# Performance work log

Measured on AMD Instinct MI355X. Metric: run time of the kernel, lower is better.

The kernel has to match this reference:

```python
import jax, jax.numpy as jnp
import numpy as np

NB, NLOC, NALL, NNEI, A_SEL = 1, 512, 640, 96, 20
N_DIM, E_DIM, A_DIM, AXIS = 128, 64, 64, 4
EDGE_INFO = 2 * N_DIM + E_DIM          # 320
SYM = AXIS * (E_DIM + N_DIM)           # 768, cal_1_dim
ANGLE = A_DIM + N_DIM + 2 * E_DIM      # 320, angle_dim


def setup_inputs() -> dict:
    key = jax.random.key(0)
    ks = jax.random.split(key, 16)
    nrm = lambda k, sh, s=1.0: jax.random.normal(k, sh, dtype=jnp.float32) * s

    def lin(k, din, dout, s=0.05):
        k1, k2 = jax.random.split(k)
        return nrm(k1, (din, dout), s), nrm(k2, (dout,), s)

    inp = {}
    inp["g1_ext"] = nrm(ks[0], (NB, NALL, N_DIM))
    inp["g2"] = nrm(ks[1], (NB, NLOC, NNEI, E_DIM))
    inp["h2"] = nrm(ks[2], (NB, NLOC, NNEI, 3))
    inp["angle_embed"] = nrm(ks[3], (NB, NLOC, A_SEL, A_SEL, A_DIM))
    inp["sw"] = jax.random.uniform(ks[4], (NB, NLOC, NNEI), dtype=jnp.float32)
    inp["a_sw"] = jax.random.uniform(ks[5], (NB, NLOC, A_SEL), dtype=jnp.float32)
    inp["w_self"], inp["b_self"] = lin(ks[6], N_DIM, N_DIM)
    inp["w_proj"] = nrm(ks[7], (E_DIM, N_DIM), 0.05)  # proj_g1g2, bias=False
    inp["w_lin1"], inp["b_lin1"] = lin(ks[8], SYM, N_DIM)
    inp["w_edge1"], inp["b_edge1"] = lin(ks[9], EDGE_INFO, N_DIM)
    inp["w_lin2"], inp["b_lin2"] = lin(ks[10], EDGE_INFO, E_DIM)
    inp["w_ang"], inp["b_ang"] = lin(ks[11], ANGLE, A_DIM)
    inp["w_ga1"], inp["b_ga1"] = lin(ks[12], ANGLE, E_DIM)
    inp["w_ga2"], inp["b_ga2"] = lin(ks[13], E_DIM, E_DIM)
    inp["nlist"] = jax.random.randint(ks[14], (NB, NLOC, NNEI), 0, NALL)
    inp["nlist_mask"] = jnp.ones((NB, NLOC, NNEI), dtype=bool)
    inp["a_nlist_mask"] = jnp.ones((NB, NLOC, A_SEL), dtype=bool)
    return inp


def _sym_op(g, h2, mask, sw, axis):
    # symmetrization_op: _cal_hg (smooth, use_sqrt_nnei) followed by _cal_grrg
    # g: nb x nloc x nnei x d, h2: nb x nloc x nnei x 3
    g = jnp.where(mask[..., None], g, 0.0) * sw[..., None]
    inv = np.float32(1.0 / np.sqrt(g.shape[2]))
    hg = jnp.einsum('blnt,blnd->bltd', h2, g) * inv
    grrg = jnp.einsum('bltd,blta->blda', hg, hg[..., :axis])  # nb x nloc x d x axis
    return grrg.reshape(grrg.shape[0], grrg.shape[1], -1)


def reference(g1_ext, g2, h2, angle_embed, sw, a_sw,
              w_self, b_self, w_proj, w_lin1, b_lin1, w_edge1, b_edge1,
              w_lin2, b_lin2, w_ang, b_ang, w_ga1, b_ga1, w_ga2, b_ga2,
              nlist, nlist_mask, a_nlist_mask):
    act = jax.nn.silu
    nb, nloc, nnei, e_dim = g2.shape
    n_dim = g1_ext.shape[-1]
    a_sel = angle_embed.shape[2]
    g1 = g1_ext[:, :nloc]
    # _make_nei_g1: gather neighbor node features, nb x nloc x nnei x n_dim
    gg1 = jnp.take_along_axis(
        g1_ext, nlist.reshape(nb, nloc * nnei, 1), axis=1
    ).reshape(nb, nloc, nnei, n_dim)
    maskf = nlist_mask[..., None]
    swf = sw[..., None]

    g1_update = [g1]
    # node self mlp
    g1_update.append(act(g1 @ w_self + b_self))
    # conv update: masked+switched gg1 times projected g2, mean over nnei
    gg1_ms = jnp.where(maskf, gg1, 0.0) * swf
    g1_update.append(jnp.sum((g2 @ w_proj) * gg1_ms, axis=2) / np.float32(nnei))
    # symmetrized axis-neuron update
    sym = jnp.concatenate(
        [_sym_op(g2, h2, nlist_mask, sw, AXIS),
         _sym_op(gg1, h2, nlist_mask, sw, AXIS)], axis=-1)
    g1_update.append(act(sym @ w_lin1 + b_lin1))
    # edge info: [tiled g1, gg1, g2] -> 2*n_dim + e_dim
    edge_info = jnp.concatenate(
        [jnp.broadcast_to(g1[:, :, None, :], (nb, nloc, nnei, n_dim)), gg1, g2],
        axis=-1)
    g1_edge = act(edge_info @ w_edge1 + b_edge1) * swf
    g1_update.append(jnp.sum(g1_edge, axis=2) / np.float32(nnei))
    # res_avg
    g1_new = sum(g1_update) / np.float32(np.sqrt(len(g1_update)))

    g2_update = [g2, act(edge_info @ w_lin2 + b_lin2)]

    # angle branch: angle_dim = a_dim + n_dim + 2*e_dim
    g2a = jnp.where(a_nlist_mask[..., None], g2[:, :, :a_sel, :], 0.0)
    ang = jnp.concatenate([
        angle_embed,
        jnp.broadcast_to(g1[:, :, None, None, :], (nb, nloc, a_sel, a_sel, n_dim)),
        jnp.broadcast_to(g2a[:, :, :, None, :], (nb, nloc, a_sel, a_sel, e_dim)),
        jnp.broadcast_to(g2a[:, :, None, :, :], (nb, nloc, a_sel, a_sel, e_dim)),
    ], axis=-1)
    a_new = (angle_embed + act(ang @ w_ang + b_ang)) / np.float32(np.sqrt(2.0))

    # angle -> edge message, switch-weighted on both angle axes, mean over one axis
    ang_w = ang * a_sw[:, :, :, None, None] * a_sw[:, :, None, :, None]
    g2_ang = jnp.sum(act(ang_w @ w_ga1 + b_ga1), axis=3) / np.float32(a_sel)
    g2_ang_full = jnp.concatenate(
        [g2_ang, jnp.zeros((nb, nloc, nnei - a_sel, e_dim), g2.dtype)], axis=2)
    g2_update.append(act(g2_ang_full @ w_ga2 + b_ga2))
    g2_new = sum(g2_update) / np.float32(np.sqrt(len(g2_update)))

    return g1_new, g2_new, h2, a_new
```

## Files before the change

kernel.cpp:

```cpp
#include <hip/hip_runtime.h>
#include <hip/hip_bf16.h>

#define NLOC 512
#define NALL 640
#define NNEI 96
#define ASEL 20
#define NDIM 128
#define EDIM 64
#define ADIM 64

typedef short bf16x8 __attribute__((ext_vector_type(8)));
typedef float f32x4 __attribute__((ext_vector_type(4)));
typedef unsigned short ushort8 __attribute__((ext_vector_type(8)));
typedef unsigned short ushort4_t __attribute__((ext_vector_type(4)));

__device__ __forceinline__ unsigned short f2bf(float f) {
    unsigned int u = __float_as_uint(f);
    unsigned int r = (u + 0x7FFFu + ((u >> 16) & 1u)) >> 16;
    return (unsigned short)r;
}
__device__ __forceinline__ float bf2f(unsigned short u) {
    return __uint_as_float(((unsigned int)u) << 16);
}
__device__ __forceinline__ float silu(float x) { return x / (1.0f + __expf(-x)); }

__device__ __forceinline__ void cvt8_store(unsigned short* dst, const float* src) {
    float4 f0 = *(const float4*)src;
    float4 f1 = *(const float4*)(src + 4);
    ushort8 v;
    v[0] = f2bf(f0.x); v[1] = f2bf(f0.y); v[2] = f2bf(f0.z); v[3] = f2bf(f0.w);
    v[4] = f2bf(f1.x); v[5] = f2bf(f1.y); v[6] = f2bf(f1.z); v[7] = f2bf(f1.w);
    *(ushort8*)dst = v;
}

__device__ __forceinline__ f32x4 red16(f32x4 v) {
#pragma unroll
    for (int m = 1; m < 16; m <<= 1) {
        v[0] += __shfl_xor(v[0], m);
        v[1] += __shfl_xor(v[1], m);
        v[2] += __shfl_xor(v[2], m);
        v[3] += __shfl_xor(v[3], m);
    }
    return v;
}

__global__ void prep_bt2(const float* __restrict__ w_ang, const float* __restrict__ w_ga1,
                         const float* __restrict__ w_edge1, const float* __restrict__ w_lin2,
                         const float* __restrict__ w_proj, const float* __restrict__ w_self,
                         unsigned short* __restrict__ bt_ae, unsigned short* __restrict__ bt_g2e,
                         unsigned short* __restrict__ bt_sm, unsigned short* __restrict__ bt_pij) {
    int idx = blockIdx.x * 256 + threadIdx.x;
    if (idx < 8192) {
        int k = idx & 63, n = idx >> 6;
        bt_ae[idx] = f2bf((n < 64) ? w_ang[k * 64 + n] : w_ga1[k * 64 + (n - 64)]);
    } else if (idx < 32768) {
        int id2 = idx - 8192;
        int k = id2 & 63, n = id2 >> 6;
        float v;
        if (n < 128)      v = w_edge1[(256 + k) * 128 + n];
        else if (n < 192) v = w_lin2[(256 + k) * 64 + (n - 128)];
        else if (n < 256) v = 0.0f;
        else              v = w_proj[k * 128 + (n - 256)];
        bt_g2e[id2] = f2bf(v);
    } else if (idx < 114688) {
        int id3 = idx - 32768;
        int k = id3 & 127, n = id3 >> 7;
        float v;
        if (n < 128)      v = w_edge1[k * 128 + n];
        else if (n < 192) v = w_lin2[k * 64 + (n - 128)];
        else if (n < 320) v = w_edge1[(128 + k) * 128 + (n - 192)];
        else if (n < 384) v = w_lin2[(128 + k) * 64 + (n - 320)];
        else if (n < 512) { int c = n - 384;
            v = (c < 64) ? w_ang[(64 + k) * 64 + c] : w_ga1[(64 + k) * 64 + (c - 64)]; }
        else              v = w_self[k * 128 + (n - 512)];
        bt_sm[id3] = f2bf(v);
    } else {
        int id4 = idx - 114688;
        int k = id4 & 63, n = id4 >> 6;
        float v;
        if (n < 128) v = (n < 64) ? w_ang[(192 + k) * 64 + n] : w_ga1[(192 + k) * 64 + (n - 64)];
        else { int c = n - 128;
            v = (c < 64) ? w_ang[(256 + k) * 64 + c] : w_ga1[(256 + k) * 64 + (c - 64)]; }
        bt_pij[id4] = f2bf(v);
    }
}

__global__ __launch_bounds__(256) void gemm_small(
    const float* __restrict__ g1_ext, const unsigned short* __restrict__ bt_sm,
    const float* __restrict__ b_self, float* __restrict__ P1a, float* __restrict__ g1self,
    float* __restrict__ E1, float* __restrict__ E2) {
    const int m0 = blockIdx.x * 128;
    const int ntile = blockIdx.y;
    __shared__ __align__(16) unsigned short Asl[128 * 136];
    __shared__ __align__(16) unsigned short Bsl[128 * 136];
    const int tid = threadIdx.x;
#pragma unroll
    for (int u = 0; u < 8; u++) {
        int g = tid + u * 256;
        int row = g >> 4, seg = g & 15;
        cvt8_store(&Asl[row * 136 + seg * 8], g1_ext + (m0 + row) * 128 + seg * 8);
        *(ushort8*)&Bsl[row * 136 + seg * 8] =
            *(const ushort8*)&bt_sm[(ntile * 128 + row) * 128 + seg * 8];
    }
    __syncthreads();
    const int lane = tid & 63, wid = tid >> 6;
    const int wr = wid >> 1, wc = wid & 1;
    const int r15 = lane & 15, kg = lane >> 4;
    f32x4 acc[4][4] = {};
#pragma unroll
    for (int h = 0; h < 4; h++) {
        bf16x8 afr[4], bfr[4];
#pragma unroll
        for (int mi = 0; mi < 4; mi++)
            afr[mi] = *(const bf16x8*)&Asl[(wr * 64 + mi * 16 + r15) * 136 + h * 32 + kg * 8];
#pragma unroll
        for (int ni = 0; ni < 4; ni++)
            bfr[ni] = *(const bf16x8*)&Bsl[(wc * 64 + ni * 16 + r15) * 136 + h * 32 + kg * 8];
#pragma unroll
        for (int mi = 0; mi < 4; mi++)
#pragma unroll
            for (int ni = 0; ni < 4; ni++)
                acc[mi][ni] = __builtin_amdgcn_mfma_f32_16x16x32_bf16(afr[mi], bfr[ni], acc[mi][ni], 0, 0, 0);
    }
#pragma unroll
    for (int mi = 0; mi < 4; mi++) {
        int rbase = m0 + wr * 64 + mi * 16 + kg * 4;
#pragma unroll
        for (int ni = 0; ni < 4; ni++) {
            int gc = ntile * 128 + wc * 64 + ni * 16 + r15;
#pragma unroll
            for (int t2 = 0; t2 < 4; t2++) {
                int a = rbase + t2;
                float z = acc[mi][ni][t2];
                if (gc < 192) { if (a < 512) E1[a * 192 + gc] = z; }
                else if (gc < 384) E2[a * 192 + (gc - 192)] = z;
                else if (gc < 512) { if (a < 512) P1a[a * 128 + (gc - 384)] = z; }
                else { if (a < 512) g1self[a * 128 + (gc - 512)] = silu(z + b_self[gc - 512]); }
            }
        }
    }
}

__global__ __launch_bounds__(256) void gemm_pij(
    const float* __restrict__ g2, const unsigned short* __restrict__ bt_pij,
    unsigned short* __restrict__ P_i, unsigned short* __restrict__ P_j,
    unsigned short* __restrict__ P_jT) {
    const int m0 = blockIdx.x * 128;
    const int ntile = blockIdx.y;
    __shared__ __align__(16) unsigned short Asl[128 * 72];
    const int tid = threadIdx.x;
#pragma unroll
    for (int u = 0; u < 4; u++) {
        int g = tid + u * 256;
        int row = g >> 3, seg = g & 7;
        int li = m0 + row, l = li / 20, i = li - l * 20;
        cvt8_store(&Asl[row * 72 + seg * 8], g2 + (l * 96 + i) * 64 + seg * 8);
    }
    __syncthreads();
    const int lane = tid & 63, wid = tid >> 6;
    const int wr = wid >> 1, wc = wid & 1;
    const int r15 = lane & 15, kg = lane >> 4;
    f32x4 acc[4][4] = {};
#pragma unroll
    for (int h = 0; h < 2; h++) {
        bf16x8 afr[4], bfr[4];
#pragma unroll
        for (int mi = 0; mi < 4; mi++)
            afr[mi] = *(const bf16x8*)&Asl[(wr * 64 + mi * 16 + r15) * 72 + h * 32 + kg * 8];
#pragma unroll
        for (int ni = 0; ni < 4; ni++)
            bfr[ni] = *(const bf16x8*)&bt_pij[(ntile * 128 + wc * 64 + ni * 16 + r15) * 64 + h * 32 + kg * 8];
#pragma unroll
        for (int mi = 0; mi < 4; mi++)
#pragma unroll
            for (int ni = 0; ni < 4; ni++)
                acc[mi][ni] = __builtin_amdgcn_mfma_f32_16x16x32_bf16(afr[mi], bfr[ni], acc[mi][ni], 0, 0, 0);
    }
    unsigned short* Pout = (ntile == 0) ? P_i : P_j;
#pragma unroll
    for (int mi = 0; mi < 4; mi++) {
        int rbase = m0 + wr * 64 + mi * 16 + kg * 4;
#pragma unroll
        for (int ni = 0; ni < 4; ni++) {
            int c = wc * 64 + ni * 16 + r15;
#pragma unroll
            for (int t2 = 0; t2 < 4; t2++) {
                unsigned short v = f2bf(acc[mi][ni][t2]);
                int li = rbase + t2;
                Pout[li * 128 + c] = v;
                if (ntile == 1) {
                    int l = li / 20, j = li - l * 20;
                    P_jT[(l * 128 + c) * 20 + j] = v;
                }
            }
        }
    }
}

__global__ void k_sym(const float* __restrict__ g1_ext, const float* __restrict__ g2,
                      const float* __restrict__ h2, const float* __restrict__ sw,
                      const int* __restrict__ nlist, const float* __restrict__ w_lin1,
                      const float* __restrict__ b_lin1, float* __restrict__ term4) {
    int l = blockIdx.x, t = threadIdx.x;
    __shared__ float h2s[96 * 3];
    __shared__ float sws[96];
    __shared__ int nls[96];
    __shared__ float hg[3 * 192];
    __shared__ float symv[768];
    __shared__ float red[128];
    if (t < 96) { sws[t] = sw[l * 96 + t]; nls[t] = nlist[l * 96 + t]; }
    for (int p = t; p < 288; p += 256) h2s[p] = h2[l * 288 + p];
    __syncthreads();
    const float inv = 0.1020620726f;
    for (int p = t; p < 576; p += 256) {
        float acc = 0.0f;
        if (p < 192) {
            int tt = p >> 6, d = p & 63;
            for (int n = 0; n < 96; n++)
                acc += h2s[n * 3 + tt] * g2[(l * 96 + n) * 64 + d] * sws[n];
            hg[tt * 192 + d] = acc * inv;
        } else {
            int q = p - 192;
            int tt = q >> 7, d = q & 127;
            for (int n = 0; n < 96; n++)
                acc += h2s[n * 3 + tt] * g1_ext[nls[n] * 128 + d] * sws[n];
            hg[tt * 192 + 64 + d] = acc * inv;
        }
    }
    __syncthreads();
    for (int p = t; p < 768; p += 256) {
        float acc = 0.0f;
        if (p < 256) {
            int d = p >> 2, a = p & 3;
            for (int tt = 0; tt < 3; tt++) acc += hg[tt * 192 + d] * hg[tt * 192 + a];
        } else {
            int q = p - 256;
            int d = q >> 2, a = q & 3;
            for (int tt = 0; tt < 3; tt++) acc += hg[tt * 192 + 64 + d] * hg[tt * 192 + 64 + a];
        }
        symv[p] = acc;
    }
    __syncthreads();
    {
        int col = t & 127, half = t >> 7;
        float acc = 0.0f;
        int k0 = half * 384;
#pragma unroll 8
        for (int k = k0; k < k0 + 384; k++) acc += symv[k] * w_lin1[k * 128 + col];
        if (half) red[col] = acc;
        __syncthreads();
        if (!half) term4[l * 128 + col] = silu(acc + red[col] + b_lin1[col]);
    }
}

__global__ __launch_bounds__(256) void angle_main(
    const float* __restrict__ ae, const unsigned short* __restrict__ bt_ae,
    const float* __restrict__ P1a, const unsigned short* __restrict__ P_i,
    const unsigned short* __restrict__ P_j, const unsigned short* __restrict__ P_jT,
    const float* __restrict__ a_sw,
    const float* __restrict__ b_ang, const float* __restrict__ b_ga1,
    float* __restrict__ g2acc, float* __restrict__ a_new_out) {
    const int m0 = blockIdx.x * 64;
    __shared__ __align__(16) unsigned short Asl[64 * 72];
    const int tid = threadIdx.x;
#pragma unroll
    for (int u = 0; u < 2; u++) {
        int g = tid + u * 256;
        int row = g >> 3, seg = g & 7;
        cvt8_store(&Asl[row * 72 + seg * 8], ae + (m0 + row) * 64 + seg * 8);
    }
    __syncthreads();
    const int lane = tid & 63, wid = tid >> 6;
    const int r15 = lane & 15, kg = lane >> 4;
    f32x4 accA[4] = {};
    f32x4 accB[4] = {};
#pragma unroll
    for (int h = 0; h < 2; h++) {
        bf16x8 afr, bfrA[4], bfrB[4];
        afr = *(const bf16x8*)&Asl[(wid * 16 + r15) * 72 + h * 32 + kg * 8];
#pragma unroll
        for (int ni = 0; ni < 4; ni++) {
            bfrA[ni] = *(const bf16x8*)&bt_ae[(ni * 16 + r15) * 64 + h * 32 + kg * 8];
            bfrB[ni] = *(const bf16x8*)&bt_ae[(64 + ni * 16 + r15) * 64 + h * 32 + kg * 8];
        }
#pragma unroll
        for (int ni = 0; ni < 4; ni++) {
            accA[ni] = __builtin_amdgcn_mfma_f32_16x16x32_bf16(bfrA[ni], afr, accA[ni], 0, 0, 0);
            accB[ni] = __builtin_amdgcn_mfma_f32_16x16x32_bf16(afr, bfrB[ni], accB[ni], 0, 0, 0);
        }
    }
    {
        int r = m0 + wid * 16 + r15;
        int l = r / 400;
        int rem = r - l * 400;
        int i = rem / 20;
        int j = rem - i * 20;
        const float* p1b = P1a + l * 128;
        const unsigned short* pib = P_i + (l * 20 + i) * 128;
        const unsigned short* pjb = P_j + (l * 20 + j) * 128;
        int lr = r - m0;
#pragma unroll
        for (int ni = 0; ni < 4; ni++) {
            int n0 = ni * 16 + kg * 4;
            f32x4 p1v = *(const f32x4*)&p1b[n0];
            ushort4_t piv = *(const ushort4_t*)&pib[n0];
            ushort4_t pjv = *(const ushort4_t*)&pjb[n0];
            ushort4_t aev = *(const ushort4_t*)&Asl[lr * 72 + n0];
            f32x4 bbv = *(const f32x4*)&b_ang[n0];
            f32x4 outv;
#pragma unroll
            for (int t2 = 0; t2 < 4; t2++) {
                float z = accA[ni][t2] + p1v[t2] + bf2f(piv[t2]) + bf2f(pjv[t2]);
                outv[t2] = (bf2f(aev[t2]) + silu(z + bbv[t2])) * 0.70710678f;
            }
            *(f32x4*)&a_new_out[r * 64 + n0] = outv;
        }
    }
    {
        int rbase = m0 + wid * 16 + kg * 4;
        int l = rbase / 400;
        int rem = rbase - l * 400;
        int i = rem / 20;
        int j0 = rem - i * 20;
        const float* p1b = P1a + l * 128;
        const unsigned short* pib = P_i + (l * 20 + i) * 128;
        float swi = a_sw[l * 20 + i];
        f32x4 swjv = *(const f32x4*)&a_sw[l * 20 + j0];
#pragma unroll
        for (int ni = 0; ni < 4; ni++) {
            int c = 64 + ni * 16 + r15;
            int cc = c - 64;
            float base = p1b[c] + bf2f(pib[c]);
            float bb = b_ga1[cc];
            ushort4_t pjtv = *(const ushort4_t*)&P_jT[(l * 128 + c) * 20 + j0];
            float part = 0.0f;
#pragma unroll
            for (int t2 = 0; t2 < 4; t2++) {
                float z = accB[ni][t2] + base + bf2f(pjtv[t2]);
                part += silu(swi * swjv[t2] * z + bb);
            }
            atomicAdd(&g2acc[(l * 20 + i) * 64 + cc], part);
        }
    }
}

__global__ void k_f2(const float* __restrict__ g2ang_acc, const float* __restrict__ w_ga2,
                     const float* __restrict__ b_ga2, float* __restrict__ yga2) {
    int l = blockIdx.x, t = threadIdx.x;
    __shared__ float gs[20 * 64];
    for (int p = t; p < 1280; p += 256) gs[p] = g2ang_acc[l * 1280 + p] * 0.05f;
    __syncthreads();
    for (int p = t; p < 1280; p += 256) {
        int i = p >> 6, c = p & 63;
        float acc = b_ga2[c];
#pragma unroll 8
        for (int k = 0; k < 64; k++) acc += gs[i * 64 + k] * w_ga2[k * 64 + c];
        yga2[l * 1280 + p] = silu(acc);
    }
}

__global__ __launch_bounds__(256) void edge_main(
    const float* __restrict__ g1_ext, const float* __restrict__ g2, const float* __restrict__ sw,
    const int* __restrict__ nlist, const unsigned short* __restrict__ bt_g2e,
    const float* __restrict__ E1, const float* __restrict__ E2,
    const float* __restrict__ b_edge1, const float* __restrict__ b_lin2,
    const float* __restrict__ b_ga2, const float* __restrict__ yga2,
    float* __restrict__ g1_acc3, float* __restrict__ g1_acc5, float* __restrict__ g2_new_out) {
    const int m0 = blockIdx.x * 128;
    const int ntile = blockIdx.y;
    __shared__ __align__(16) unsigned short Asl[128 * 72];
    const int tid = threadIdx.x;
#pragma unroll
    for (int u = 0; u < 4; u++) {
        int g = tid + u * 256;
        int row = g >> 3, seg = g & 7;
        cvt8_store(&Asl[row * 72 + seg * 8], g2 + (m0 + row) * 64 + seg * 8);
    }
    __syncthreads();
    const int lane = tid & 63, wid = tid >> 6;
    const int r15 = lane & 15, kg = lane >> 4;
    if (ntile == 1) {
        f32x4 acc[2][4] = {};
#pragma unroll
        for (int h = 0; h < 2; h++) {
            bf16x8 afr[2], bfr[4];
#pragma unroll
            for (int mi = 0; mi < 2; mi++)
                afr[mi] = *(const bf16x8*)&Asl[(wid * 32 + mi * 16 + r15) * 72 + h * 32 + kg * 8];
#pragma unroll
            for (int ni = 0; ni < 4; ni++)
                bfr[ni] = *(const bf16x8*)&bt_g2e[(128 + ni * 16 + r15) * 64 + h * 32 + kg * 8];
#pragma unroll
            for (int mi = 0; mi < 2; mi++)
#pragma unroll
                for (int ni = 0; ni < 4; ni++)
                    acc[mi][ni] = __builtin_amdgcn_mfma_f32_16x16x32_bf16(bfr[ni], afr[mi], acc[mi][ni], 0, 0, 0);
        }
#pragma unroll
        for (int mi = 0; mi < 2; mi++) {
            int r = m0 + wid * 32 + mi * 16 + r15;
            int l = r / 96;
            int nn = r - l * 96;
            const float* e1 = E1 + l * 192 + 128;
            const float* e2 = E2 + nlist[r] * 192 + 128;
            bool hasyg = (nn < ASEL);
            const float* yg = yga2 + (l * 20 + nn) * 64;
            int lr = r - m0;
#pragma unroll
            for (int ni = 0; ni < 4; ni++) {
                int n0 = ni * 16 + kg * 4;
                f32x4 e1v = *(const f32x4*)&e1[n0];
                f32x4 e2v = *(const f32x4*)&e2[n0];
                f32x4 bbv = *(const f32x4*)&b_lin2[n0];
                f32x4 bg2 = *(const f32x4*)&b_ga2[n0];
                ushort4_t g2v = *(const ushort4_t*)&Asl[lr * 72 + n0];
                f32x4 outv;
#pragma unroll
                for (int t2 = 0; t2 < 4; t2++) {
                    float z = acc[mi][ni][t2] + e1v[t2] + e2v[t2];
                    float y = silu(z + bbv[t2]);
                    float ygv = hasyg ? yg[n0 + t2] : silu(bg2[t2]);
                    outv[t2] = (bf2f(g2v[t2]) + y + ygv) * 0.57735027f;
                }
                *(f32x4*)&g2_new_out[r * 64 + n0] = outv;
            }
        }
    } else {
        const int bn = (ntile == 0) ? 0 : 256;
        f32x4 acc[2][8] = {};
#pragma unroll
        for (int h = 0; h < 2; h++) {
            bf16x8 afr[2], bfr[8];
#pragma unroll
            for (int mi = 0; mi < 2; mi++)
                afr[mi] = *(const bf16x8*)&Asl[(wid * 32 + mi * 16 + r15) * 72 + h * 32 + kg * 8];
#pragma unroll
            for (int ni = 0; ni < 8; ni++)
                bfr[ni] = *(const bf16x8*)&bt_g2e[(bn + ni * 16 + r15) * 64 + h * 32 + kg * 8];
#pragma unroll
            for (int mi = 0; mi < 2; mi++)
#pragma unroll
                for (int ni = 0; ni < 8; ni++)
                    acc[mi][ni] = __builtin_amdgcn_mfma_f32_16x16x32_bf16(bfr[ni], afr[mi], acc[mi][ni], 0, 0, 0);
        }
#pragma unroll
        for (int mi = 0; mi < 2; mi++) {
            int r = m0 + wid * 32 + mi * 16 + r15;
            int l = r / 96;
            float swr = sw[r];
            int nr = nlist[r];
            if (ntile == 0) {
                const float* e1 = E1 + l * 192;
                const float* e2 = E2 + nr * 192;
#pragma unroll
                for (int ni = 0; ni < 8; ni++) {
                    int n0 = ni * 16 + kg * 4;
                    f32x4 e1v = *(const f32x4*)&e1[n0];
                    f32x4 e2v = *(const f32x4*)&e2[n0];
                    f32x4 bbv = *(const f32x4*)&b_edge1[n0];
                    f32x4 p;
#pragma unroll
                    for (int t2 = 0; t2 < 4; t2++)
                        p[t2] = silu(acc[mi][ni][t2] + e1v[t2] + e2v[t2] + bbv[t2]) * swr;
                    p = red16(p);
                    if (r15 == 0) {
#pragma unroll
                        for (int t2 = 0; t2 < 4; t2++)
                            atomicAdd(&g1_acc5[l * 128 + n0 + t2], p[t2]);
                    }
                }
            } else {
                const float* gv = g1_ext + nr * 128;
#pragma unroll
                for (int ni = 0; ni < 8; ni++) {
                    int n0 = ni * 16 + kg * 4;
                    f32x4 g4 = *(const f32x4*)&gv[n0];
                    f32x4 p;
#pragma unroll
                    for (int t2 = 0; t2 < 4; t2++)
                        p[t2] = acc[mi][ni][t2] * g4[t2] * swr;
                    p = red16(p);
                    if (r15 == 0) {
#pragma unroll
                        for (int t2 = 0; t2 < 4; t2++)
                            atomicAdd(&g1_acc3[l * 128 + n0 + t2], p[t2]);
                    }
                }
            }
        }
    }
}

__global__ void k_f1(const float* __restrict__ g1_ext, const float* __restrict__ g1self,
                     const float* __restrict__ acc3, const float* __restrict__ term4,
                     const float* __restrict__ acc5, const float* __restrict__ h2,
                     float* __restrict__ out_g1, float* __restrict__ out_h2) {
    int idx = blockIdx.x * 256 + threadIdx.x;
    float v = g1_ext[idx] + g1self[idx] + acc3[idx] * (1.0f / 96.0f) + term4[idx] +
              acc5[idx] * (1.0f / 96.0f);
    out_g1[idx] = v * 0.4472135955f;
    if (idx < 36864)
        *(float4*)&out_h2[idx * 4] = *(const float4*)&h2[idx * 4];
}

extern "C" void kernel_launch(void* const* d_in, const int* in_sizes, int n_in,
                              void* d_out, int out_size, void* d_ws, size_t ws_size,
                              hipStream_t stream) {
    if (n_in < 22 || in_sizes[0] != 81920 || in_sizes[3] != 13107200) return;
    const float* g1_ext = (const float*)d_in[0];
    const float* g2     = (const float*)d_in[1];
    const float* h2     = (const float*)d_in[2];
    const float* ae     = (const float*)d_in[3];
    const float* sw     = (const float*)d_in[4];
    const float* a_sw   = (const float*)d_in[5];
    const float* w_self = (const float*)d_in[6];
    const float* b_self = (const float*)d_in[7];
    const float* w_proj = (const float*)d_in[8];
    const float* w_lin1 = (const float*)d_in[9];
    const float* b_lin1 = (const float*)d_in[10];
    const float* w_edge1= (const float*)d_in[11];
    const float* b_edge1= (const float*)d_in[12];
    const float* w_lin2 = (const float*)d_in[13];
    const float* b_lin2 = (const float*)d_in[14];
    const float* w_ang  = (const float*)d_in[15];
    const float* b_ang  = (const float*)d_in[16];
    const float* w_ga1  = (const float*)d_in[17];
    const float* b_ga1  = (const float*)d_in[18];
    const float* w_ga2  = (const float*)d_in[19];
    const float* b_ga2  = (const float*)d_in[20];
    const int*   nlist  = (const int*)d_in[21];

    float* ws = (float*)d_ws;
    unsigned short* bt_ae  = (unsigned short*)(ws);
    unsigned short* bt_g2e = (unsigned short*)(ws + 4096);
    unsigned short* bt_sm  = (unsigned short*)(ws + 16384);
    unsigned short* bt_pij = (unsigned short*)(ws + 57344);
    float* P1a    = ws + 65536;
    float* E1     = ws + 131072;
    float* E2     = ws + 229376;
    unsigned short* P_i = (unsigned short*)(ws + 352256);
    unsigned short* P_j = (unsigned short*)(ws + 1007616);
    float* g1self = ws + 1662976;
    float* term4  = ws + 1728512;
    float* yga2   = ws + 1794048;
    float* acc3   = ws + 2449408;
    float* acc5   = ws + 2514944;
    float* g2acc  = ws + 2580480;
    unsigned short* P_jT = (unsigned short*)(ws + 3235840);
    if (ws_size < (size_t)3563520 * sizeof(float)) return;

    float* out = (float*)d_out;
    float* out_g1 = out;
    float* out_g2 = out + 65536;
    float* out_h2 = out + 3211264;
    float* out_an = out + 3358720;

    hipMemsetAsync(acc3, 0, (65536 + 65536 + 655360) * sizeof(float), stream);

    prep_bt2<<<512, 256, 0, stream>>>(w_ang, w_ga1, w_edge1, w_lin2, w_proj, w_self,
                                      bt_ae, bt_g2e, bt_sm, bt_pij);
    gemm_small<<<dim3(5, 5), 256, 0, stream>>>(g1_ext, bt_sm, b_self, P1a, g1self, E1, E2);
    gemm_pij<<<dim3(80, 2), 256, 0, stream>>>(g2, bt_pij, P_i, P_j, P_jT);
    k_sym<<<512, 256, 0, stream>>>(g1_ext, g2, h2, sw, nlist, w_lin1, b_lin1, term4);
    angle_main<<<3200, 256, 0, stream>>>(ae, bt_ae, P1a, P_i, P_j, P_jT, a_sw, b_ang, b_ga1,
                                         g2acc, out_an);
    k_f2<<<512, 256, 0, stream>>>(g2acc, w_ga2, b_ga2, yga2);
    edge_main<<<dim3(384, 3), 256, 0, stream>>>(g1_ext, g2, sw, nlist, bt_g2e, E1, E2,
                                                b_edge1, b_lin2, b_ga2, yga2,
                                                acc3, acc5, out_g2);
    k_f1<<<256, 256, 0, stream>>>(g1_ext, g1self, acc3, term4, acc5, h2, out_g1, out_h2);
}
```

Measured before the change: 166.9 us.

## Restructure angle kernel rows so each wave owns full i-rows, drop atomics

```diff
diff --git a/kernel.cpp b/kernel.cpp
--- a/kernel.cpp
+++ b/kernel.cpp
@@ -253,95 +253,105 @@
     }
 }
 
-__global__ __launch_bounds__(256) void angle_main(
+__global__ __launch_bounds__(128) void angle_main(
     const float* __restrict__ ae, const unsigned short* __restrict__ bt_ae,
     const float* __restrict__ P1a, const unsigned short* __restrict__ P_i,
     const unsigned short* __restrict__ P_j, const unsigned short* __restrict__ P_jT,
     const float* __restrict__ a_sw,
     const float* __restrict__ b_ang, const float* __restrict__ b_ga1,
     float* __restrict__ g2acc, float* __restrict__ a_new_out) {
-    const int m0 = blockIdx.x * 64;
-    __shared__ __align__(16) unsigned short Asl[64 * 72];
+    const int m0 = blockIdx.x * 160;
+    __shared__ __align__(16) unsigned short Asl[160 * 72];
     const int tid = threadIdx.x;
 #pragma unroll
-    for (int u = 0; u < 2; u++) {
-        int g = tid + u * 256;
-        int row = g >> 3, seg = g & 7;
-        cvt8_store(&Asl[row * 72 + seg * 8], ae + (m0 + row) * 64 + seg * 8);
-    }
-    __syncthreads();
-    const int lane = tid & 63, wid = tid >> 6;
+    for (int u = 0; u < 10; u++) {
+        int g = tid + u * 128;
+        int slot = g >> 3, seg = g & 7;
+        int chunk = slot / 80, s = slot - chunk * 80;
+        int t = s >> 4, w16 = s & 15;
+        int kg2 = w16 >> 2, t2s = w16 & 3;
+        int grow = m0 + chunk * 80 + kg2 * 20 + t * 4 + t2s;
+        cvt8_store(&Asl[slot * 72 + seg * 8], ae + grow * 64 + seg * 8);
+    }
+    __syncthreads();
+    const int lane = tid & 63, w = tid >> 6;
     const int r15 = lane & 15, kg = lane >> 4;
-    f32x4 accA[4] = {};
-    f32x4 accB[4] = {};
-#pragma unroll
-    for (int h = 0; h < 2; h++) {
-        bf16x8 afr, bfrA[4], bfrB[4];
-        afr = *(const bf16x8*)&Asl[(wid * 16 + r15) * 72 + h * 32 + kg * 8];
-#pragma unroll
-        for (int ni = 0; ni < 4; ni++) {
-            bfrA[ni] = *(const bf16x8*)&bt_ae[(ni * 16 + r15) * 64 + h * 32 + kg * 8];
-            bfrB[ni] = *(const bf16x8*)&bt_ae[(64 + ni * 16 + r15) * 64 + h * 32 + kg * 8];
-        }
-#pragma unroll
-        for (int ni = 0; ni < 4; ni++) {
-            accA[ni] = __builtin_amdgcn_mfma_f32_16x16x32_bf16(bfrA[ni], afr, accA[ni], 0, 0, 0);
-            accB[ni] = __builtin_amdgcn_mfma_f32_16x16x32_bf16(afr, bfrB[ni], accB[ni], 0, 0, 0);
-        }
-    }
-    {
-        int r = m0 + wid * 16 + r15;
-        int l = r / 400;
-        int rem = r - l * 400;
-        int i = rem / 20;
-        int j = rem - i * 20;
-        const float* p1b = P1a + l * 128;
-        const unsigned short* pib = P_i + (l * 20 + i) * 128;
-        const unsigned short* pjb = P_j + (l * 20 + j) * 128;
-        int lr = r - m0;
-#pragma unroll
-        for (int ni = 0; ni < 4; ni++) {
-            int n0 = ni * 16 + kg * 4;
-            f32x4 p1v = *(const f32x4*)&p1b[n0];
-            ushort4_t piv = *(const ushort4_t*)&pib[n0];
-            ushort4_t pjv = *(const ushort4_t*)&pjb[n0];
-            ushort4_t aev = *(const ushort4_t*)&Asl[lr * 72 + n0];
-            f32x4 bbv = *(const f32x4*)&b_ang[n0];
-            f32x4 outv;
-#pragma unroll
-            for (int t2 = 0; t2 < 4; t2++) {
-                float z = accA[ni][t2] + p1v[t2] + bf2f(piv[t2]) + bf2f(pjv[t2]);
-                outv[t2] = (bf2f(aev[t2]) + silu(z + bbv[t2])) * 0.70710678f;
-            }
-            *(f32x4*)&a_new_out[r * 64 + n0] = outv;
-        }
-    }
-    {
-        int rbase = m0 + wid * 16 + kg * 4;
-        int l = rbase / 400;
-        int rem = rbase - l * 400;
-        int i = rem / 20;
-        int j0 = rem - i * 20;
-        const float* p1b = P1a + l * 128;
-        const unsigned short* pib = P_i + (l * 20 + i) * 128;
-        float swi = a_sw[l * 20 + i];
-        f32x4 swjv = *(const f32x4*)&a_sw[l * 20 + j0];
-#pragma unroll
-        for (int ni = 0; ni < 4; ni++) {
-            int c = 64 + ni * 16 + r15;
-            int cc = c - 64;
-            float base = p1b[c] + bf2f(pib[c]);
-            float bb = b_ga1[cc];
-            ushort4_t pjtv = *(const ushort4_t*)&P_jT[(l * 128 + c) * 20 + j0];
-            float part = 0.0f;
-#pragma unroll
-            for (int t2 = 0; t2 < 4; t2++) {
-                float z = accB[ni][t2] + base + bf2f(pjtv[t2]);
-                part += silu(swi * swjv[t2] * z + bb);
-            }
-            atomicAdd(&g2acc[(l * 20 + i) * 64 + cc], part);
-        }
-    }
+    const int cb = m0 + w * 80;
+    const int l = cb / 400;
+    const int i0 = (cb - l * 400) / 20;
+    const int kgA = r15 >> 2, t2A = r15 & 3;
+    const int iA = i0 + kgA;
+    f32x4 p1vA[4], bbvA[4];
+    ushort4_t pivA[4];
+#pragma unroll
+    for (int ni = 0; ni < 4; ni++) {
+        int n0 = ni * 16 + kg * 4;
+        p1vA[ni] = *(const f32x4*)&P1a[l * 128 + n0];
+        pivA[ni] = *(const ushort4_t*)&P_i[(l * 20 + iA) * 128 + n0];
+        bbvA[ni] = *(const f32x4*)&b_ang[n0];
+    }
+    const int iB = i0 + kg;
+    const float swi = a_sw[l * 20 + iB];
+    float baseB[4], bbB[4];
+#pragma unroll
+    for (int ni = 0; ni < 4; ni++) {
+        int c = 64 + ni * 16 + r15;
+        baseB[ni] = P1a[l * 128 + c] + bf2f(P_i[(l * 20 + iB) * 128 + c]);
+        bbB[ni] = b_ga1[ni * 16 + r15];
+    }
+    f32x4 part = {0.0f, 0.0f, 0.0f, 0.0f};
+#pragma unroll
+    for (int t = 0; t < 5; t++) {
+        f32x4 accA[4] = {};
+        f32x4 accB[4] = {};
+#pragma unroll
+        for (int h = 0; h < 2; h++) {
+            bf16x8 afr = *(const bf16x8*)&Asl[(w * 80 + t * 16 + r15) * 72 + h * 32 + kg * 8];
+#pragma unroll
+            for (int ni = 0; ni < 4; ni++) {
+                bf16x8 bfrA = *(const bf16x8*)&bt_ae[(ni * 16 + r15) * 64 + h * 32 + kg * 8];
+                bf16x8 bfrB = *(const bf16x8*)&bt_ae[(64 + ni * 16 + r15) * 64 + h * 32 + kg * 8];
+                accA[ni] = __builtin_amdgcn_mfma_f32_16x16x32_bf16(bfrA, afr, accA[ni], 0, 0, 0);
+                accB[ni] = __builtin_amdgcn_mfma_f32_16x16x32_bf16(afr, bfrB, accB[ni], 0, 0, 0);
+            }
+        }
+        {
+            int jA = 4 * t + t2A;
+            int r = cb + kgA * 20 + jA;
+            int lsl = w * 80 + t * 16 + r15;
+#pragma unroll
+            for (int ni = 0; ni < 4; ni++) {
+                int n0 = ni * 16 + kg * 4;
+                ushort4_t pjv = *(const ushort4_t*)&P_j[(l * 20 + jA) * 128 + n0];
+                ushort4_t aev = *(const ushort4_t*)&Asl[lsl * 72 + n0];
+                f32x4 outv;
+#pragma unroll
+                for (int t2 = 0; t2 < 4; t2++) {
+                    float z = accA[ni][t2] + p1vA[ni][t2] + bf2f(pivA[ni][t2]) + bf2f(pjv[t2]);
+                    outv[t2] = (bf2f(aev[t2]) + silu(z + bbvA[ni][t2])) * 0.70710678f;
+                }
+                *(f32x4*)&a_new_out[r * 64 + n0] = outv;
+            }
+        }
+        {
+            f32x4 swj4 = *(const f32x4*)&a_sw[l * 20 + 4 * t];
+#pragma unroll
+            for (int ni = 0; ni < 4; ni++) {
+                int c = 64 + ni * 16 + r15;
+                ushort4_t pjtv = *(const ushort4_t*)&P_jT[(l * 128 + c) * 20 + 4 * t];
+                float p = 0.0f;
+#pragma unroll
+                for (int t2 = 0; t2 < 4; t2++) {
+                    float z = accB[ni][t2] + baseB[ni] + bf2f(pjtv[t2]);
+                    p += silu(swi * swj4[t2] * z + bbB[ni]);
+                }
+                part[ni] += p;
+            }
+        }
+    }
+#pragma unroll
+    for (int ni = 0; ni < 4; ni++)
+        g2acc[(l * 20 + iB) * 64 + ni * 16 + r15] = part[ni];
 }
 
 __global__ void k_f2(const float* __restrict__ g2ang_acc, const float* __restrict__ w_ga2,
@@ -555,14 +565,14 @@
     float* out_h2 = out + 3211264;
     float* out_an = out + 3358720;
 
-    hipMemsetAsync(acc3, 0, (65536 + 65536 + 655360) * sizeof(float), stream);
+    hipMemsetAsync(acc3, 0, (65536 + 65536) * sizeof(float), stream);
 
     prep_bt2<<<512, 256, 0, stream>>>(w_ang, w_ga1, w_edge1, w_lin2, w_proj, w_self,
                                       bt_ae, bt_g2e, bt_sm, bt_pij);
     gemm_small<<<dim3(5, 5), 256, 0, stream>>>(g1_ext, bt_sm, b_self, P1a, g1self, E1, E2);
     gemm_pij<<<dim3(80, 2), 256, 0, stream>>>(g2, bt_pij, P_i, P_j, P_jT);
     k_sym<<<512, 256, 0, stream>>>(g1_ext, g2, h2, sw, nlist, w_lin1, b_lin1, term4);
-    angle_main<<<3200, 256, 0, stream>>>(ae, bt_ae, P1a, P_i, P_j, P_jT, a_sw, b_ang, b_ga1,
+    angle_main<<<1280, 128, 0, stream>>>(ae, bt_ae, P1a, P_i, P_j, P_jT, a_sw, b_ang, b_ga1,
                                          g2acc, out_an);
     k_f2<<<512, 256, 0, stream>>>(g2acc, w_ga2, b_ga2, yga2);
     edge_main<<<dim3(384, 3), 256, 0, stream>>>(g1_ext, g2, sw, nlist, bt_g2e, E1, E2,
```

Measured after the change: 169.3 us. Within noise of the previous version (+1.5%).
